# Performance work log

Hardware: AMD Instinct MI355X
Metric: run time of the kernel (lower is better)

Reference implementation:

```python
import jax, jax.numpy as jnp
import numpy as np
from jax import lax

START_IDX = 0
STOP_IDX = 1


def _forward_alg(feats_lbt, mask_lb, transitions):
    # feats_lbt: [L, B, T], mask_lb: [L, B], transitions[i, j] = score(j -> i)
    L, B, T = feats_lbt.shape
    init = jnp.full((B, T), -10000.0, dtype=feats_lbt.dtype).at[:, START_IDX].set(0.0)

    def step(fv, xs):
        feat, m = xs  # feat: [B, T], m: [B]
        # scores[b, next, prev] = fv[b, prev] + transitions[next, prev] + feat[b, next]
        scores = fv[:, None, :] + transitions[None, :, :] + feat[:, :, None]
        alphas = jax.nn.logsumexp(scores, axis=-1)  # [B, T]
        fv = jnp.where(m[:, None] > 0, alphas, fv)
        return fv, None

    fv, _ = lax.scan(step, init, (feats_lbt, mask_lb))
    terminal = fv + transitions[STOP_IDX][None, :]
    return jax.nn.logsumexp(terminal, axis=-1)  # [B]


def _score_sentence(feats_lbt, tags_bl, mask_lb, transitions):
    L, B, T = feats_lbt.shape
    start_col = jnp.full((B, 1), START_IDX, dtype=tags_bl.dtype)
    tags_ext = jnp.concatenate([start_col, tags_bl], axis=-1)  # [B, L+1]
    # transition scores along the gold path: [B, L]
    trans = transitions[tags_ext[:, 1:], tags_ext[:, :-1]]
    # emission scores: feats is [L, B, T] -> gather per-position gold tag
    emit = jnp.take_along_axis(
        feats_lbt, tags_bl.T[:, :, None], axis=-1
    )[:, :, 0]  # [L, B]
    step_scores = (trans.T + emit) * (mask_lb > 0)  # [L, B]
    score = step_scores.sum(axis=0)  # [B]
    lengths = mask_lb.sum(axis=0).astype(jnp.int32)  # [B]
    last_tag = tags_ext[jnp.arange(B), lengths]
    score = score + transitions[STOP_IDX, last_tag]
    return score


def setup_inputs() -> dict:
    key = jax.random.key(0)
    k1, k2, k3 = jax.random.split(key, 3)
    B, L, T = 256, 2048, 32
    efeats = jax.random.normal(k1, (B, L, T), dtype=jnp.float32)
    mask = jnp.ones((B, L), dtype=jnp.float32)
    tgt = jax.random.randint(k2, (B, L), 0, T, dtype=jnp.int32)
    transitions = jax.random.normal(k3, (T, T), dtype=jnp.float32)
    return {"efeats": efeats, "mask": mask, "tgt": tgt, "transitions": transitions}


def reference(efeats, mask, tgt, transitions):
    B, L = mask.shape
    mask_lb = mask.T  # [L, B]
    feats_lbt = jnp.transpose(efeats, (1, 0, 2))  # [L, B, T]
    forward_score = _forward_alg(feats_lbt, mask_lb, transitions)
    gold_score = _score_sentence(feats_lbt, tgt, mask_lb, transitions)
    loss = (forward_score - gold_score).sum() / B
    return loss
```

## Files before the change

kernel.cpp:

```cpp
#include <hip/hip_runtime.h>

#define B_SZ 256
#define L_SZ 2048
#define T_SZ 32
#define START_IDX 0
#define STOP_IDX 1

#define CLEN 64
#define NPAIR 32
#define NSLOT 8
#define NMAT_SEQ 4
#define NBLK_TOT (B_SZ * NMAT_SEQ)

#define FB_NCH 16
#define FB_CLEN 128

#define SCALE_LN 4.1588830833596718565f

typedef __attribute__((ext_vector_type(8))) short bf16x8;
typedef __attribute__((ext_vector_type(4))) float f32x4;
typedef __attribute__((ext_vector_type(2))) float f32x2;

__device__ __forceinline__ unsigned fau(float f){ union{float f; unsigned u;} v; v.f=f; return v.u; }
__device__ __forceinline__ float uaf(unsigned u){ union{unsigned u; float f;} v; v.u=u; return v.f; }
__device__ __forceinline__ int pack_trunc(float lo, float hi){
  return (int)__builtin_amdgcn_perm(fau(hi), fau(lo), 0x07060302u);
}
__device__ __forceinline__ bf16x8 frag_of(const int* p){
  union{ int i[4]; bf16x8 v; } u;
  u.i[0]=p[0]; u.i[1]=p[1]; u.i[2]=p[2]; u.i[3]=p[3];
  return u.v;
}

__device__ __forceinline__ void mfma4(bf16x8 A0, bf16x8 A1, bf16x8 B0, bf16x8 B1,
                                      f32x4& c00, f32x4& c01, f32x4& c10, f32x4& c11)
{
  const f32x4 z = {0.f,0.f,0.f,0.f};
  asm("s_nop 1\n\t"
      "v_mfma_f32_16x16x32_bf16 %0, %4, %5, %8\n\t"
      "v_mfma_f32_16x16x32_bf16 %1, %4, %6, %8\n\t"
      "v_mfma_f32_16x16x32_bf16 %2, %7, %5, %8\n\t"
      "v_mfma_f32_16x16x32_bf16 %3, %7, %6, %8\n\t"
      "s_nop 7\n\t"
      "s_nop 7"
      : "=&v"(c00), "=&v"(c01), "=&v"(c10), "=&v"(c11)
      : "v"(A0), "v"(B0), "v"(B1), "v"(A1), "v"(z));
}

__global__ void zero_kernel(float* out){ if(threadIdx.x==0) out[0]=0.f; }

__device__ __forceinline__ int mat_prod(const unsigned short* L, const unsigned short* Rt,
                                        unsigned short* dst, bool writeT, int lane)
{
  const int g = lane >> 4, c16 = lane & 15;
  const int ko = 8*g;
  bf16x8 A0 = *(const bf16x8*)(L  + (c16*T_SZ      + ko));
  bf16x8 A1 = *(const bf16x8*)(L  + ((16+c16)*T_SZ + ko));
  bf16x8 B0 = *(const bf16x8*)(Rt + (c16*T_SZ      + ko));
  bf16x8 B1 = *(const bf16x8*)(Rt + ((16+c16)*T_SZ + ko));
  f32x4 q00,q01,q10,q11;
  mfma4(A0, A1, B0, B1, q00, q01, q10, q11);

  unsigned mb = (unsigned)__builtin_amdgcn_readfirstlane((int)fau(q00[0]));
  int e = (int)((mb>>23)&255u) - 127;
  float r = uaf((unsigned)(127-e)<<23);
  #pragma unroll
  for (int i=0;i<4;++i){ q00[i]*=r; q01[i]*=r; q10[i]*=r; q11[i]*=r; }

  if (!writeT){
    #pragma unroll
    for (int reg=0; reg<4; ++reg){
      int x0 = 4*g + reg, x1 = 16 + 4*g + reg;
      dst[x0*T_SZ + c16]      = (unsigned short)(fau(q00[reg])>>16);
      dst[x0*T_SZ + 16 + c16] = (unsigned short)(fau(q01[reg])>>16);
      dst[x1*T_SZ + c16]      = (unsigned short)(fau(q10[reg])>>16);
      dst[x1*T_SZ + 16 + c16] = (unsigned short)(fau(q11[reg])>>16);
    }
  } else {
    #pragma unroll
    for (int rp=0; rp<2; ++rp){
      int xb0 = 4*g + 2*rp, xb1 = 16 + 4*g + 2*rp;
      *(int*)&dst[c16*T_SZ + xb0]        = pack_trunc(q00[2*rp], q00[2*rp+1]);
      *(int*)&dst[(16+c16)*T_SZ + xb0]   = pack_trunc(q01[2*rp], q01[2*rp+1]);
      *(int*)&dst[c16*T_SZ + xb1]        = pack_trunc(q10[2*rp], q10[2*rp+1]);
      *(int*)&dst[(16+c16)*T_SZ + xb1]   = pack_trunc(q11[2*rp], q11[2*rp+1]);
    }
  }
  return e;
}

__global__ __launch_bounds__(512, 8) void crf_chunk_kernel(
    const float* __restrict__ efeats, const float* __restrict__ mask,
    const int* __restrict__ tgt, const float* __restrict__ trans,
    unsigned short* __restrict__ wsM, int* __restrict__ wsE,
    float* __restrict__ wsG, float* __restrict__ wsL,
    float* __restrict__ out)
{
  __shared__ float s_trans[T_SZ*T_SZ];
  __shared__ float s_d[8][128];
  __shared__ unsigned short s_tree[NSLOT][T_SZ*T_SZ];
  __shared__ int   s_et[NSLOT];
  __shared__ float s_gd[8], s_ml[8];

  const int tid  = threadIdx.x;
  const int w    = tid >> 6;
  const int lane = tid & 63;
  const int g    = lane >> 4;
  const int c16  = lane & 15;

  const int b  = blockIdx.x >> 2;
  const int q  = blockIdx.x & 3;
  const int c  = q*NSLOT + w;
  const int l0 = c * CLEN;

  if (blockIdx.x == 0 && tid == 0) out[0] = 0.f;

  s_trans[tid]     = trans[tid];
  s_trans[tid+512] = trans[tid+512];
  __syncthreads();

  bf16x8 A0f, A1f;
  {
    int a0i[4], a1i[4];
    #pragma unroll
    for (int I=0; I<2; ++I){
      int row = 8*(c16>>2) + 4*I + (c16&3);
      float e[8];
      #pragma unroll
      for (int j=0;j<8;++j) e[j] = __expf(s_trans[row*T_SZ + 8*g + j]);
      int* dst = I ? a1i : a0i;
      #pragma unroll
      for (int p=0;p<4;++p) dst[p] = pack_trunc(e[2*p], e[2*p+1]);
    }
    A0f = frag_of(a0i); A1f = frag_of(a1i);
  }

  int b0[4], b1[4];
  #pragma unroll
  for (int p=0;p<4;++p){
    int s0 = 8*g + 2*p, s1 = s0+1;
    unsigned lo = (s0==c16)?0x3f80u:0u, hi = (s1==c16)?0x3f80u:0u;
    b0[p] = (int)(lo | (hi<<16));
    lo = (s0==16+c16)?0x3f80u:0u; hi = (s1==16+c16)?0x3f80u:0u;
    b1[p] = (int)(lo | (hi<<16));
  }

  const long fbase = ((long)b * L_SZ) * T_SZ;
  const int  mbase = b*L_SZ + l0;

  float mA = mask[mbase + lane];
  int   tA = tgt [mbase + lane];
  int   tpA = (l0 + lane == 0) ? START_IDX : tgt[mbase + lane - 1];

  float emA = efeats[fbase + (long)(l0+lane)*T_SZ + tA];
  float gl = (mA > 0.f) ? (s_trans[tA*T_SZ + tpA] + emA) : 0.f;
  float ml = mA;
  #pragma unroll
  for (int off=32; off>0; off>>=1){ gl += __shfl_xor(gl, off, 64); ml += __shfl_xor(ml, off, 64); }

  unsigned long long mb0 = __ballot(mA > 0.f);

  const float* fpt = efeats + fbase + (long)l0*T_SZ;
  float* s_dw = &s_d[w][0];

  float fq[4];
  #pragma unroll
  for (int i=1; i<=4; ++i) fq[i&3] = fpt[i*64 + lane];
  s_dw[lane] = __expf(fpt[lane] - SCALE_LN);

  if (mb0 == ~0ull){
    #pragma unroll 4
    for (int p=0; p<NPAIR; ++p){
      s_dw[((p+1)&1)*64 + lane] = __expf(fq[(p+1)&3] - SCALE_LN);
      int np = p+5; np = (np > NPAIR-1) ? (NPAIR-1) : np;
      fq[(p+1)&3] = fpt[np*64 + lane];
      const float* dbase = &s_dw[(p&1)*64];
      #pragma unroll
      for (int h=0; h<2; ++h){
        f32x4 c00,c01,c10,c11;
        mfma4(A0f, A1f, frag_of(b0), frag_of(b1), c00,c01,c10,c11);

        const float4* dv = (const float4*)(dbase + h*32);
        float4 dl = dv[2*g], dh2 = dv[2*g+1];
        f32x2 q0={c00[0],c00[1]}; q0 *= (f32x2){dl.x,dl.y};
        f32x2 q1={c00[2],c00[3]}; q1 *= (f32x2){dl.z,dl.w};
        f32x2 q2={c01[0],c01[1]}; q2 *= (f32x2){dl.x,dl.y};
        f32x2 q3={c01[2],c01[3]}; q3 *= (f32x2){dl.z,dl.w};
        f32x2 q4={c10[0],c10[1]}; q4 *= (f32x2){dh2.x,dh2.y};
        f32x2 q5={c10[2],c10[3]}; q5 *= (f32x2){dh2.z,dh2.w};
        f32x2 q6={c11[0],c11[1]}; q6 *= (f32x2){dh2.x,dh2.y};
        f32x2 q7={c11[2],c11[3]}; q7 *= (f32x2){dh2.z,dh2.w};

        b0[0]=pack_trunc(q0[0],q0[1]); b0[1]=pack_trunc(q1[0],q1[1]);
        b0[2]=pack_trunc(q4[0],q4[1]); b0[3]=pack_trunc(q5[0],q5[1]);
        b1[0]=pack_trunc(q2[0],q2[1]); b1[1]=pack_trunc(q3[0],q3[1]);
        b1[2]=pack_trunc(q6[0],q6[1]); b1[3]=pack_trunc(q7[0],q7[1]);
      }
    }
  } else {
    for (int p=0; p<NPAIR; ++p){
      s_dw[((p+1)&1)*64 + lane] = __expf(fq[(p+1)&3] - SCALE_LN);
      int np = p+5; if (np > NPAIR-1) np = NPAIR-1;
      fq[(p+1)&3] = fpt[np*64 + lane];
      const float* dbase = &s_dw[(p&1)*64];
      #pragma unroll
      for (int h=0; h<2; ++h){
        int t = 2*p + h;
        if ((mb0 >> t) & 1ull){
          f32x4 c00,c01,c10,c11;
          mfma4(A0f, A1f, frag_of(b0), frag_of(b1), c00,c01,c10,c11);

          const float4* dv = (const float4*)(dbase + h*32);
          float4 dl = dv[2*g], dh2 = dv[2*g+1];
          float f0=dl.x, f1=dl.y, f2=dl.z, f3=dl.w;
          float f4=dh2.x, f5=dh2.y, f6=dh2.z, f7=dh2.w;

          c00[0]*=f0; c00[1]*=f1; c00[2]*=f2; c00[3]*=f3;
          c01[0]*=f0; c01[1]*=f1; c01[2]*=f2; c01[3]*=f3;
          c10[0]*=f4; c10[1]*=f5; c10[2]*=f6; c10[3]*=f7;
          c11[0]*=f4; c11[1]*=f5; c11[2]*=f6; c11[3]*=f7;

          b0[0]=pack_trunc(c00[0],c00[1]); b0[1]=pack_trunc(c00[2],c00[3]);
          b0[2]=pack_trunc(c10[0],c10[1]); b0[3]=pack_trunc(c10[2],c10[3]);
          b1[0]=pack_trunc(c01[0],c01[1]); b1[1]=pack_trunc(c01[2],c01[3]);
          b1[2]=pack_trunc(c11[0],c11[1]); b1[3]=pack_trunc(c11[2],c11[3]);
        }
      }
    }
  }

  {
    unsigned short* S = &s_tree[w][0];
    if ((w & 1) == 0){
      #pragma unroll
      for (int p=0;p<4;++p){
        int s = 8*g + 2*p;
        *(int*)&S[c16*T_SZ + s]      = b0[p];
        *(int*)&S[(16+c16)*T_SZ + s] = b1[p];
      }
    } else {
      #pragma unroll
      for (int p=0;p<4;++p){
        int s = 8*g + 2*p;
        S[s*T_SZ + c16]          = (unsigned short)(b0[p] & 0xffff);
        S[(s+1)*T_SZ + c16]      = (unsigned short)(((unsigned)b0[p])>>16);
        S[s*T_SZ + 16 + c16]     = (unsigned short)(b1[p] & 0xffff);
        S[(s+1)*T_SZ + 16 + c16] = (unsigned short)(((unsigned)b1[p])>>16);
      }
    }
  }
  if (lane==0){
    s_et[w] = 6 * __popcll(mb0);
    s_gd[w] = gl; s_ml[w] = ml;
  }
  __syncthreads();

  if (w < 4){
    int e = mat_prod(&s_tree[2*w][0], &s_tree[2*w+1][0], &s_tree[2*w][0], (w&1)!=0, lane);
    if (lane==0) s_et[2*w] = s_et[2*w] + s_et[2*w+1] + e;
  }
  __syncthreads();
  if (w < 2){
    int e = mat_prod(&s_tree[4*w][0], &s_tree[4*w+2][0], &s_tree[4*w][0], (w&1)!=0, lane);
    if (lane==0) s_et[4*w] = s_et[4*w] + s_et[4*w+2] + e;
  }
  __syncthreads();
  if (w == 0){
    int e = mat_prod(&s_tree[0][0], &s_tree[4][0], &s_tree[0][0], false, lane);
    if (lane==0) s_et[0] = s_et[0] + s_et[4] + e;
  }
  __syncthreads();

  const int bid = blockIdx.x;
  ((int*)(wsM + (long)bid*(T_SZ*T_SZ)))[tid] = ((const int*)&s_tree[0][0])[tid];
  if (tid == 0){
    wsE[bid] = s_et[0];
    float gs=0.f, ls=0.f;
    #pragma unroll
    for (int i=0;i<8;++i){ gs += s_gd[i]; ls += s_ml[i]; }
    wsG[bid] = gs; wsL[bid] = ls;
  }
}

__global__ __launch_bounds__(64) void crf_combine_kernel(
    const unsigned short* __restrict__ wsM, const int* __restrict__ wsE,
    const float* __restrict__ wsG, const float* __restrict__ wsL,
    const int* __restrict__ tgt, const float* __restrict__ trans,
    float* __restrict__ out)
{
  __shared__ unsigned short sM[NMAT_SEQ*T_SZ*T_SZ];
  __shared__ float s_v[T_SZ];

  const int tid = threadIdx.x;
  const int b   = blockIdx.x;

  const uint4* src = (const uint4*)(wsM + (long)b*NMAT_SEQ*T_SZ*T_SZ);
  #pragma unroll
  for (int i=0;i<NMAT_SEQ*4;++i) ((uint4*)sM)[tid + i*64] = src[tid + i*64];
  __syncthreads();

  const int s = tid & 31;
  float v = (s==START_IDX)?1.f:0.f;
  int E = 0;
  #pragma unroll
  for (int j=0; j<NMAT_SEQ; ++j){
    if (tid < 32) s_v[s] = v;
    __syncthreads();
    const unsigned short* M = &sM[j*T_SZ*T_SZ];
    float u = 0.f;
    #pragma unroll 8
    for (int x=0; x<T_SZ; ++x){
      float mv = uaf(((unsigned)M[x*T_SZ + s])<<16);
      u = fmaf(mv, s_v[x], u);
    }
    unsigned ub = (unsigned)__builtin_amdgcn_readfirstlane((int)fau(u));
    int eu = (int)((ub>>23)&255u)-127;
    E += wsE[b*NMAT_SEQ + j] + eu;
    v = u * uaf((unsigned)(127-eu)<<23);
    __syncthreads();
  }
  float term = v * __expf(trans[STOP_IDX*T_SZ + s]);
  #pragma unroll
  for (int off=16; off>0; off>>=1) term += __shfl_xor(term, off, 32);
  float fwd = (float)E * 0.69314718055994530942f + __logf(term);

  if (tid == 0){
    float gp = 0.f, lp = 0.f;
    #pragma unroll
    for (int j=0;j<NMAT_SEQ;++j){ gp += wsG[b*NMAT_SEQ+j]; lp += wsL[b*NMAT_SEQ+j]; }
    int len = (int)lp;
    int last_tag = (len==0)? START_IDX : tgt[b*L_SZ + len-1];
    float goldT = gp + trans[STOP_IDX*T_SZ + last_tag];
    atomicAdd(out, (fwd - goldT) * (1.0f/B_SZ));
  }
}

__global__ __launch_bounds__(1024) void crf_loss_kernel(
    const float* __restrict__ efeats, const float* __restrict__ mask,
    const int* __restrict__ tgt, const float* __restrict__ trans,
    float* __restrict__ out)
{
  __shared__ float s_trans[T_SZ*T_SZ];
  __shared__ float s_d[FB_NCH][T_SZ];
  __shared__ unsigned short s_M[FB_NCH][T_SZ*T_SZ];
  __shared__ int   s_es[FB_NCH];
  __shared__ float s_gd[FB_NCH];
  __shared__ float s_mlv[FB_NCH];

  const int tid  = threadIdx.x;
  const int b    = blockIdx.x;
  const int w    = tid >> 6;
  const int lane = tid & 63;
  const int g    = lane >> 4;
  const int c16  = lane & 15;
  const int i32  = lane & 31;

  s_trans[tid] = trans[tid];
  __syncthreads();

  int a0[4], a1[4];
  #pragma unroll
  for (int I=0; I<2; ++I){
    int row = 8*(c16>>2) + 4*I + (c16&3);
    float e[8];
    #pragma unroll
    for (int j=0;j<8;++j) e[j] = __expf(s_trans[row*T_SZ + 8*g + j]);
    int* dst = I ? a1 : a0;
    #pragma unroll
    for (int p=0;p<4;++p) dst[p] = pack_trunc(e[2*p], e[2*p+1]);
  }

  int b0[4], b1[4];
  #pragma unroll
  for (int p=0;p<4;++p){
    int s0 = 8*g + 2*p, s1 = s0+1;
    unsigned lo = (s0==c16)?0x3f80u:0u, hi = (s1==c16)?0x3f80u:0u;
    b0[p] = (int)(lo | (hi<<16));
    lo = (s0==16+c16)?0x3f80u:0u; hi = (s1==16+c16)?0x3f80u:0u;
    b1[p] = (int)(lo | (hi<<16));
  }

  const int l0 = w * FB_CLEN;
  const long fbase = ((long)b * L_SZ) * T_SZ;

  float fqv[4];
  #pragma unroll
  for (int i=0;i<4;++i) fqv[i] = efeats[fbase + (long)(l0+i)*T_SZ + i32];

  int   tA = tgt [b*L_SZ + l0 + lane];
  int   tB = tgt [b*L_SZ + l0 + 64 + lane];
  float mA = mask[b*L_SZ + l0 + lane];
  float mB = mask[b*L_SZ + l0 + 64 + lane];
  int prev = (l0==0) ? START_IDX : tgt[b*L_SZ + l0 - 1];

  int esum = 0;
  float gold = 0.f, mlen = 0.f;
  const f32x4 zf = {0.f,0.f,0.f,0.f};

  #pragma unroll 4
  for (int t=0; t<FB_CLEN; ++t){
    float fcur = fqv[t&3];
    int lpf = l0 + t + 4; lpf = (lpf < L_SZ) ? lpf : (L_SZ-1);
    fqv[t&3] = efeats[fbase + (long)lpf*T_SZ + i32];

    float mk  = uaf((unsigned)__builtin_amdgcn_readlane((int)fau((t<64)?mA:mB), t&63));
    int   cur = __builtin_amdgcn_readlane((t<64)?tA:tB, t&63);
    mlen += mk;

    if (mk > 0.f){
      if (lane < 32) s_d[w][lane] = __expf(fcur);

      f32x4 c00 = __builtin_amdgcn_mfma_f32_16x16x32_bf16(frag_of(a0), frag_of(b0), zf, 0,0,0);
      f32x4 c01 = __builtin_amdgcn_mfma_f32_16x16x32_bf16(frag_of(a0), frag_of(b1), zf, 0,0,0);
      f32x4 c10 = __builtin_amdgcn_mfma_f32_16x16x32_bf16(frag_of(a1), frag_of(b0), zf, 0,0,0);
      f32x4 c11 = __builtin_amdgcn_mfma_f32_16x16x32_bf16(frag_of(a1), frag_of(b1), zf, 0,0,0);

      const float4* dv = (const float4*)(&s_d[w][0]);
      float4 dl = dv[2*g], dh = dv[2*g+1];
      float f0=dl.x, f1=dl.y, f2=dl.z, f3=dl.w;
      float f4=dh.x, f5=dh.y, f6=dh.z, f7=dh.w;

      float m00 = c00[0]*f0;
      unsigned mb = (unsigned)__builtin_amdgcn_readfirstlane((int)fau(m00));
      int e = (int)((mb>>23)&255u) - 127;
      esum += e;
      float r = uaf((unsigned)(127-e)<<23);
      f0*=r; f1*=r; f2*=r; f3*=r; f4*=r; f5*=r; f6*=r; f7*=r;

      c00[0]*=f0; c00[1]*=f1; c00[2]*=f2; c00[3]*=f3;
      c01[0]*=f0; c01[1]*=f1; c01[2]*=f2; c01[3]*=f3;
      c10[0]*=f4; c10[1]*=f5; c10[2]*=f6; c10[3]*=f7;
      c11[0]*=f4; c11[1]*=f5; c11[2]*=f6; c11[3]*=f7;

      b0[0]=pack_trunc(c00[0],c00[1]); b0[1]=pack_trunc(c00[2],c00[3]);
      b0[2]=pack_trunc(c10[0],c10[1]); b0[3]=pack_trunc(c10[2],c10[3]);
      b1[0]=pack_trunc(c01[0],c01[1]); b1[1]=pack_trunc(c01[2],c01[3]);
      b1[2]=pack_trunc(c11[0],c11[1]); b1[3]=pack_trunc(c11[2],c11[3]);

      float tp   = s_trans[cur*T_SZ + prev];
      float emit = uaf((unsigned)__builtin_amdgcn_readlane((int)fau(fcur), cur));
      gold += tp + emit;
    }
    prev = cur;
  }

  #pragma unroll
  for (int p=0;p<4;++p){
    int s = 8*g + 2*p;
    *(int*)((char*)(&s_M[w][0]) + (((long)(c16   )*T_SZ + s) * 2)) = b0[p];
    *(int*)((char*)(&s_M[w][0]) + (((long)(16+c16)*T_SZ + s) * 2)) = b1[p];
  }
  if (lane==0){ s_es[w]=esum; s_gd[w]=gold; s_mlv[w]=mlen; }
  __syncthreads();

  if (w==0){
    int s = i32;
    float v = (s==START_IDX)?1.f:0.f;
    int E = 0;
    for (int c=0;c<FB_NCH;++c){
      float u=0.f;
      #pragma unroll 8
      for (int k=0;k<T_SZ;++k){
        float mv = uaf(((unsigned)s_M[c][k*T_SZ + s])<<16);
        float vk = uaf((unsigned)__builtin_amdgcn_readlane((int)fau(v), k));
        u = fmaf(mv, vk, u);
      }
      unsigned ub = (unsigned)__builtin_amdgcn_readfirstlane((int)fau(u));
      int eu = (int)((ub>>23)&255u)-127;
      E += s_es[c] + eu;
      v = u * uaf((unsigned)(127-eu)<<23);
    }
    float term = v * __expf(s_trans[STOP_IDX*T_SZ + s]);
    #pragma unroll
    for (int off=16; off>0; off>>=1) term += __shfl_xor(term, off, 32);
    float fwd = (float)E * 0.69314718055994530942f + __logf(term);

    float gp = (s<FB_NCH)? s_gd[s] : 0.f;
    float lp = (s<FB_NCH)? s_mlv[s] : 0.f;
    #pragma unroll
    for (int off=16; off>0; off>>=1){ gp += __shfl_xor(gp, off, 32); lp += __shfl_xor(lp, off, 32); }
    int len = (int)lp;
    int last_tag = (len==0)? START_IDX : tgt[b*L_SZ + (len-1)];
    float goldT = gp + s_trans[STOP_IDX*T_SZ + last_tag];
    if (tid==0) atomicAdd(out, (fwd - goldT) * (1.0f/B_SZ));
  }
}

extern "C" void kernel_launch(void* const* d_in, const int* in_sizes, int n_in,
                              void* d_out, int out_size, void* d_ws, size_t ws_size,
                              hipStream_t stream)
{
  const float* efeats = (const float*)d_in[0];
  const float* mask   = (const float*)d_in[1];
  const int*   tgt    = (const int*)d_in[2];
  const float* trans  = (const float*)d_in[3];
  float* out = (float*)d_out;

  const size_t needM = (size_t)NBLK_TOT * T_SZ * T_SZ * 2;
  const size_t need  = needM + (size_t)NBLK_TOT * 12;

  if (ws_size >= need){
    unsigned short* wsM = (unsigned short*)d_ws;
    char* p = (char*)d_ws + needM;
    int*   wsE = (int*)p;
    float* wsG = (float*)(p + (size_t)NBLK_TOT*4);
    float* wsL = (float*)(p + (size_t)NBLK_TOT*8);
    crf_chunk_kernel<<<dim3(NBLK_TOT), dim3(512), 0, stream>>>(
        efeats, mask, tgt, trans, wsM, wsE, wsG, wsL, out);
    crf_combine_kernel<<<dim3(B_SZ), dim3(64), 0, stream>>>(
        wsM, wsE, wsG, wsL, tgt, trans, out);
  } else {
    zero_kernel<<<dim3(1), dim3(64), 0, stream>>>(out);
    crf_loss_kernel<<<dim3(B_SZ), dim3(1024), 0, stream>>>(efeats, mask, tgt, trans, out);
  }
}
```

Measured before the change: 139.4 us.

## Interleave two sequence chunks per wavefront to overlap MFMA dependency chains

Each wavefront now advances two independent 64-step chunks of the recurrence at once. A new 8-MFMA inline-asm block issues both chunks' matrix products back to back, so the fixed s_nop padding is shared between them. The chunk kernel now launches 256-thread blocks with half as many waves, and the first level of the tree reduction is done by every wave. The combine kernel's shared-memory copy loop is also halved so it matches the actual size of sM, which the old loop overran. The cost is more registers per wave and fewer waves for the scheduler to switch between.

```diff
diff --git a/kernel.cpp b/kernel.cpp
--- a/kernel.cpp
+++ b/kernel.cpp
@@ -47,6 +47,28 @@
       : "v"(A0), "v"(B0), "v"(B1), "v"(A1), "v"(z));
 }
 
+__device__ __forceinline__ void mfma8(bf16x8 A0, bf16x8 A1,
+                                      bf16x8 Ba0, bf16x8 Ba1, bf16x8 Bb0, bf16x8 Bb1,
+                                      f32x4& a00, f32x4& a01, f32x4& a10, f32x4& a11,
+                                      f32x4& b00, f32x4& b01, f32x4& b10, f32x4& b11)
+{
+  const f32x4 z = {0.f,0.f,0.f,0.f};
+  asm("s_nop 1\n\t"
+      "v_mfma_f32_16x16x32_bf16 %0, %8, %10, %14\n\t"
+      "v_mfma_f32_16x16x32_bf16 %1, %8, %11, %14\n\t"
+      "v_mfma_f32_16x16x32_bf16 %2, %9, %10, %14\n\t"
+      "v_mfma_f32_16x16x32_bf16 %3, %9, %11, %14\n\t"
+      "v_mfma_f32_16x16x32_bf16 %4, %8, %12, %14\n\t"
+      "v_mfma_f32_16x16x32_bf16 %5, %8, %13, %14\n\t"
+      "v_mfma_f32_16x16x32_bf16 %6, %9, %12, %14\n\t"
+      "v_mfma_f32_16x16x32_bf16 %7, %9, %13, %14\n\t"
+      "s_nop 7\n\t"
+      "s_nop 7"
+      : "=&v"(a00), "=&v"(a01), "=&v"(a10), "=&v"(a11),
+        "=&v"(b00), "=&v"(b01), "=&v"(b10), "=&v"(b11)
+      : "v"(A0), "v"(A1), "v"(Ba0), "v"(Ba1), "v"(Bb0), "v"(Bb1), "v"(z));
+}
+
 __global__ void zero_kernel(float* out){ if(threadIdx.x==0) out[0]=0.f; }
 
 __device__ __forceinline__ int mat_prod(const unsigned short* L, const unsigned short* Rt,
@@ -89,7 +111,7 @@
   return e;
 }
 
-__global__ __launch_bounds__(512, 8) void crf_chunk_kernel(
+__global__ __launch_bounds__(256, 4) void crf_chunk_kernel(
     const float* __restrict__ efeats, const float* __restrict__ mask,
     const int* __restrict__ tgt, const float* __restrict__ trans,
     unsigned short* __restrict__ wsM, int* __restrict__ wsE,
@@ -97,10 +119,10 @@
     float* __restrict__ out)
 {
   __shared__ float s_trans[T_SZ*T_SZ];
-  __shared__ float s_d[8][128];
+  __shared__ float s_d[4][256];
   __shared__ unsigned short s_tree[NSLOT][T_SZ*T_SZ];
   __shared__ int   s_et[NSLOT];
-  __shared__ float s_gd[8], s_ml[8];
+  __shared__ float s_gd[4], s_ml[4];
 
   const int tid  = threadIdx.x;
   const int w    = tid >> 6;
@@ -110,13 +132,13 @@
 
   const int b  = blockIdx.x >> 2;
   const int q  = blockIdx.x & 3;
-  const int c  = q*NSLOT + w;
-  const int l0 = c * CLEN;
+  const int l0A = q*(NSLOT*CLEN) + (2*w)*CLEN;
+  const int l0B = l0A + CLEN;
 
   if (blockIdx.x == 0 && tid == 0) out[0] = 0.f;
 
-  s_trans[tid]     = trans[tid];
-  s_trans[tid+512] = trans[tid+512];
+  #pragma unroll
+  for (int i=0;i<4;++i) s_trans[tid + i*256] = trans[tid + i*256];
   __syncthreads();
 
   bf16x8 A0f, A1f;
@@ -135,127 +157,174 @@
     A0f = frag_of(a0i); A1f = frag_of(a1i);
   }
 
-  int b0[4], b1[4];
+  int b0a[4], b1a[4], b0b[4], b1b[4];
   #pragma unroll
   for (int p=0;p<4;++p){
     int s0 = 8*g + 2*p, s1 = s0+1;
     unsigned lo = (s0==c16)?0x3f80u:0u, hi = (s1==c16)?0x3f80u:0u;
-    b0[p] = (int)(lo | (hi<<16));
+    b0a[p] = (int)(lo | (hi<<16));  b0b[p] = b0a[p];
     lo = (s0==16+c16)?0x3f80u:0u; hi = (s1==16+c16)?0x3f80u:0u;
-    b1[p] = (int)(lo | (hi<<16));
+    b1a[p] = (int)(lo | (hi<<16));  b1b[p] = b1a[p];
   }
 
   const long fbase = ((long)b * L_SZ) * T_SZ;
-  const int  mbase = b*L_SZ + l0;
-
-  float mA = mask[mbase + lane];
-  int   tA = tgt [mbase + lane];
-  int   tpA = (l0 + lane == 0) ? START_IDX : tgt[mbase + lane - 1];
-
-  float emA = efeats[fbase + (long)(l0+lane)*T_SZ + tA];
-  float gl = (mA > 0.f) ? (s_trans[tA*T_SZ + tpA] + emA) : 0.f;
-  float ml = mA;
+  const int  mbA = b*L_SZ + l0A;
+  const int  mbB = b*L_SZ + l0B;
+
+  float mA = mask[mbA + lane];
+  float mB = mask[mbB + lane];
+  int   tA = tgt [mbA + lane];
+  int   tB = tgt [mbB + lane];
+  int   tpA = (l0A + lane == 0) ? START_IDX : tgt[mbA + lane - 1];
+  int   tpB = tgt[mbB + lane - 1];
+
+  float emA = efeats[fbase + (long)(l0A+lane)*T_SZ + tA];
+  float emB = efeats[fbase + (long)(l0B+lane)*T_SZ + tB];
+  float gl = ((mA > 0.f) ? (s_trans[tA*T_SZ + tpA] + emA) : 0.f)
+           + ((mB > 0.f) ? (s_trans[tB*T_SZ + tpB] + emB) : 0.f);
+  float ml = mA + mB;
   #pragma unroll
   for (int off=32; off>0; off>>=1){ gl += __shfl_xor(gl, off, 64); ml += __shfl_xor(ml, off, 64); }
 
-  unsigned long long mb0 = __ballot(mA > 0.f);
-
-  const float* fpt = efeats + fbase + (long)l0*T_SZ;
-  float* s_dw = &s_d[w][0];
-
-  float fq[4];
-  #pragma unroll
-  for (int i=1; i<=4; ++i) fq[i&3] = fpt[i*64 + lane];
-  s_dw[lane] = __expf(fpt[lane] - SCALE_LN);
-
-  if (mb0 == ~0ull){
-    #pragma unroll 4
+  unsigned long long mba = __ballot(mA > 0.f);
+  unsigned long long mbb = __ballot(mB > 0.f);
+
+  const float* fptA = efeats + fbase + (long)l0A*T_SZ;
+  const float* fptB = efeats + fbase + (long)l0B*T_SZ;
+  float* s_dwA = &s_d[w][0];
+  float* s_dwB = &s_d[w][128];
+
+  float fqa[4], fqb[4];
+  #pragma unroll
+  for (int i=1; i<=4; ++i){ fqa[i&3] = fptA[i*64 + lane]; fqb[i&3] = fptB[i*64 + lane]; }
+  s_dwA[lane] = __expf(fptA[lane] - SCALE_LN);
+  s_dwB[lane] = __expf(fptB[lane] - SCALE_LN);
+
+  if ((mba & mbb) == ~0ull){
+    #pragma unroll 2
     for (int p=0; p<NPAIR; ++p){
-      s_dw[((p+1)&1)*64 + lane] = __expf(fq[(p+1)&3] - SCALE_LN);
+      s_dwA[((p+1)&1)*64 + lane] = __expf(fqa[(p+1)&3] - SCALE_LN);
+      s_dwB[((p+1)&1)*64 + lane] = __expf(fqb[(p+1)&3] - SCALE_LN);
       int np = p+5; np = (np > NPAIR-1) ? (NPAIR-1) : np;
-      fq[(p+1)&3] = fpt[np*64 + lane];
-      const float* dbase = &s_dw[(p&1)*64];
+      fqa[(p+1)&3] = fptA[np*64 + lane];
+      fqb[(p+1)&3] = fptB[np*64 + lane];
+      const float* dbA = &s_dwA[(p&1)*64];
+      const float* dbB = &s_dwB[(p&1)*64];
       #pragma unroll
       for (int h=0; h<2; ++h){
-        f32x4 c00,c01,c10,c11;
-        mfma4(A0f, A1f, frag_of(b0), frag_of(b1), c00,c01,c10,c11);
-
-        const float4* dv = (const float4*)(dbase + h*32);
-        float4 dl = dv[2*g], dh2 = dv[2*g+1];
-        f32x2 q0={c00[0],c00[1]}; q0 *= (f32x2){dl.x,dl.y};
-        f32x2 q1={c00[2],c00[3]}; q1 *= (f32x2){dl.z,dl.w};
-        f32x2 q2={c01[0],c01[1]}; q2 *= (f32x2){dl.x,dl.y};
-        f32x2 q3={c01[2],c01[3]}; q3 *= (f32x2){dl.z,dl.w};
-        f32x2 q4={c10[0],c10[1]}; q4 *= (f32x2){dh2.x,dh2.y};
-        f32x2 q5={c10[2],c10[3]}; q5 *= (f32x2){dh2.z,dh2.w};
-        f32x2 q6={c11[0],c11[1]}; q6 *= (f32x2){dh2.x,dh2.y};
-        f32x2 q7={c11[2],c11[3]}; q7 *= (f32x2){dh2.z,dh2.w};
-
-        b0[0]=pack_trunc(q0[0],q0[1]); b0[1]=pack_trunc(q1[0],q1[1]);
-        b0[2]=pack_trunc(q4[0],q4[1]); b0[3]=pack_trunc(q5[0],q5[1]);
-        b1[0]=pack_trunc(q2[0],q2[1]); b1[1]=pack_trunc(q3[0],q3[1]);
-        b1[2]=pack_trunc(q6[0],q6[1]); b1[3]=pack_trunc(q7[0],q7[1]);
+        f32x4 cA00,cA01,cA10,cA11, cB00,cB01,cB10,cB11;
+        mfma8(A0f, A1f, frag_of(b0a), frag_of(b1a), frag_of(b0b), frag_of(b1b),
+              cA00,cA01,cA10,cA11, cB00,cB01,cB10,cB11);
+
+        const float4* dvA = (const float4*)(dbA + h*32);
+        const float4* dvB = (const float4*)(dbB + h*32);
+        float4 dlA = dvA[2*g], dhA = dvA[2*g+1];
+        float4 dlB = dvB[2*g], dhB = dvB[2*g+1];
+
+        {
+          f32x2 q0={cA00[0],cA00[1]}; q0 *= (f32x2){dlA.x,dlA.y};
+          f32x2 q1={cA00[2],cA00[3]}; q1 *= (f32x2){dlA.z,dlA.w};
+          f32x2 q2={cA01[0],cA01[1]}; q2 *= (f32x2){dlA.x,dlA.y};
+          f32x2 q3={cA01[2],cA01[3]}; q3 *= (f32x2){dlA.z,dlA.w};
+          f32x2 q4={cA10[0],cA10[1]}; q4 *= (f32x2){dhA.x,dhA.y};
+          f32x2 q5={cA10[2],cA10[3]}; q5 *= (f32x2){dhA.z,dhA.w};
+          f32x2 q6={cA11[0],cA11[1]}; q6 *= (f32x2){dhA.x,dhA.y};
+          f32x2 q7={cA11[2],cA11[3]}; q7 *= (f32x2){dhA.z,dhA.w};
+          b0a[0]=pack_trunc(q0[0],q0[1]); b0a[1]=pack_trunc(q1[0],q1[1]);
+          b0a[2]=pack_trunc(q4[0],q4[1]); b0a[3]=pack_trunc(q5[0],q5[1]);
+          b1a[0]=pack_trunc(q2[0],q2[1]); b1a[1]=pack_trunc(q3[0],q3[1]);
+          b1a[2]=pack_trunc(q6[0],q6[1]); b1a[3]=pack_trunc(q7[0],q7[1]);
+        }
+        {
+          f32x2 q0={cB00[0],cB00[1]}; q0 *= (f32x2){dlB.x,dlB.y};
+          f32x2 q1={cB00[2],cB00[3]}; q1 *= (f32x2){dlB.z,dlB.w};
+          f32x2 q2={cB01[0],cB01[1]}; q2 *= (f32x2){dlB.x,dlB.y};
+          f32x2 q3={cB01[2],cB01[3]}; q3 *= (f32x2){dlB.z,dlB.w};
+          f32x2 q4={cB10[0],cB10[1]}; q4 *= (f32x2){dhB.x,dhB.y};
+          f32x2 q5={cB10[2],cB10[3]}; q5 *= (f32x2){dhB.z,dhB.w};
+          f32x2 q6={cB11[0],cB11[1]}; q6 *= (f32x2){dhB.x,dhB.y};
+          f32x2 q7={cB11[2],cB11[3]}; q7 *= (f32x2){dhB.z,dhB.w};
+          b0b[0]=pack_trunc(q0[0],q0[1]); b0b[1]=pack_trunc(q1[0],q1[1]);
+          b0b[2]=pack_trunc(q4[0],q4[1]); b0b[3]=pack_trunc(q5[0],q5[1]);
+          b1b[0]=pack_trunc(q2[0],q2[1]); b1b[1]=pack_trunc(q3[0],q3[1]);
+          b1b[2]=pack_trunc(q6[0],q6[1]); b1b[3]=pack_trunc(q7[0],q7[1]);
+        }
       }
     }
   } else {
     for (int p=0; p<NPAIR; ++p){
-      s_dw[((p+1)&1)*64 + lane] = __expf(fq[(p+1)&3] - SCALE_LN);
+      s_dwA[((p+1)&1)*64 + lane] = __expf(fqa[(p+1)&3] - SCALE_LN);
+      s_dwB[((p+1)&1)*64 + lane] = __expf(fqb[(p+1)&3] - SCALE_LN);
       int np = p+5; if (np > NPAIR-1) np = NPAIR-1;
-      fq[(p+1)&3] = fpt[np*64 + lane];
-      const float* dbase = &s_dw[(p&1)*64];
+      fqa[(p+1)&3] = fptA[np*64 + lane];
+      fqb[(p+1)&3] = fptB[np*64 + lane];
+      const float* dbA = &s_dwA[(p&1)*64];
+      const float* dbB = &s_dwB[(p&1)*64];
       #pragma unroll
       for (int h=0; h<2; ++h){
         int t = 2*p + h;
-        if ((mb0 >> t) & 1ull){
-          f32x4 c00,c01,c10,c11;
-          mfma4(A0f, A1f, frag_of(b0), frag_of(b1), c00,c01,c10,c11);
-
-          const float4* dv = (const float4*)(dbase + h*32);
-          float4 dl = dv[2*g], dh2 = dv[2*g+1];
+        f32x4 cA00,cA01,cA10,cA11, cB00,cB01,cB10,cB11;
+        mfma8(A0f, A1f, frag_of(b0a), frag_of(b1a), frag_of(b0b), frag_of(b1b),
+              cA00,cA01,cA10,cA11, cB00,cB01,cB10,cB11);
+
+        if ((mba >> t) & 1ull){
+          const float4* dvA = (const float4*)(dbA + h*32);
+          float4 dl = dvA[2*g], dh2 = dvA[2*g+1];
           float f0=dl.x, f1=dl.y, f2=dl.z, f3=dl.w;
           float f4=dh2.x, f5=dh2.y, f6=dh2.z, f7=dh2.w;
-
-          c00[0]*=f0; c00[1]*=f1; c00[2]*=f2; c00[3]*=f3;
-          c01[0]*=f0; c01[1]*=f1; c01[2]*=f2; c01[3]*=f3;
-          c10[0]*=f4; c10[1]*=f5; c10[2]*=f6; c10[3]*=f7;
-          c11[0]*=f4; c11[1]*=f5; c11[2]*=f6; c11[3]*=f7;
-
-          b0[0]=pack_trunc(c00[0],c00[1]); b0[1]=pack_trunc(c00[2],c00[3]);
-          b0[2]=pack_trunc(c10[0],c10[1]); b0[3]=pack_trunc(c10[2],c10[3]);
-          b1[0]=pack_trunc(c01[0],c01[1]); b1[1]=pack_trunc(c01[2],c01[3]);
-          b1[2]=pack_trunc(c11[0],c11[1]); b1[3]=pack_trunc(c11[2],c11[3]);
+          cA00[0]*=f0; cA00[1]*=f1; cA00[2]*=f2; cA00[3]*=f3;
+          cA01[0]*=f0; cA01[1]*=f1; cA01[2]*=f2; cA01[3]*=f3;
+          cA10[0]*=f4; cA10[1]*=f5; cA10[2]*=f6; cA10[3]*=f7;
+          cA11[0]*=f4; cA11[1]*=f5; cA11[2]*=f6; cA11[3]*=f7;
+          b0a[0]=pack_trunc(cA00[0],cA00[1]); b0a[1]=pack_trunc(cA00[2],cA00[3]);
+          b0a[2]=pack_trunc(cA10[0],cA10[1]); b0a[3]=pack_trunc(cA10[2],cA10[3]);
+          b1a[0]=pack_trunc(cA01[0],cA01[1]); b1a[1]=pack_trunc(cA01[2],cA01[3]);
+          b1a[2]=pack_trunc(cA11[0],cA11[1]); b1a[3]=pack_trunc(cA11[2],cA11[3]);
+        }
+        if ((mbb >> t) & 1ull){
+          const float4* dvB = (const float4*)(dbB + h*32);
+          float4 dl = dvB[2*g], dh2 = dvB[2*g+1];
+          float f0=dl.x, f1=dl.y, f2=dl.z, f3=dl.w;
+          float f4=dh2.x, f5=dh2.y, f6=dh2.z, f7=dh2.w;
+          cB00[0]*=f0; cB00[1]*=f1; cB00[2]*=f2; cB00[3]*=f3;
+          cB01[0]*=f0; cB01[1]*=f1; cB01[2]*=f2; cB01[3]*=f3;
+          cB10[0]*=f4; cB10[1]*=f5; cB10[2]*=f6; cB10[3]*=f7;
+          cB11[0]*=f4; cB11[1]*=f5; cB11[2]*=f6; cB11[3]*=f7;
+          b0b[0]=pack_trunc(cB00[0],cB00[1]); b0b[1]=pack_trunc(cB00[2],cB00[3]);
+          b0b[2]=pack_trunc(cB10[0],cB10[1]); b0b[3]=pack_trunc(cB10[2],cB10[3]);
+          b1b[0]=pack_trunc(cB01[0],cB01[1]); b1b[1]=pack_trunc(cB01[2],cB01[3]);
+          b1b[2]=pack_trunc(cB11[0],cB11[1]); b1b[3]=pack_trunc(cB11[2],cB11[3]);
         }
       }
     }
   }
 
   {
-    unsigned short* S = &s_tree[w][0];
-    if ((w & 1) == 0){
-      #pragma unroll
-      for (int p=0;p<4;++p){
-        int s = 8*g + 2*p;
-        *(int*)&S[c16*T_SZ + s]      = b0[p];
-        *(int*)&S[(16+c16)*T_SZ + s] = b1[p];
-      }
-    } else {
-      #pragma unroll
-      for (int p=0;p<4;++p){
-        int s = 8*g + 2*p;
-        S[s*T_SZ + c16]          = (unsigned short)(b0[p] & 0xffff);
-        S[(s+1)*T_SZ + c16]      = (unsigned short)(((unsigned)b0[p])>>16);
-        S[s*T_SZ + 16 + c16]     = (unsigned short)(b1[p] & 0xffff);
-        S[(s+1)*T_SZ + 16 + c16] = (unsigned short)(((unsigned)b1[p])>>16);
-      }
+    unsigned short* S = &s_tree[2*w][0];
+    #pragma unroll
+    for (int p=0;p<4;++p){
+      int s = 8*g + 2*p;
+      *(int*)&S[c16*T_SZ + s]      = b0a[p];
+      *(int*)&S[(16+c16)*T_SZ + s] = b1a[p];
+    }
+    unsigned short* St = &s_tree[2*w+1][0];
+    #pragma unroll
+    for (int p=0;p<4;++p){
+      int s = 8*g + 2*p;
+      St[s*T_SZ + c16]          = (unsigned short)(b0b[p] & 0xffff);
+      St[(s+1)*T_SZ + c16]      = (unsigned short)(((unsigned)b0b[p])>>16);
+      St[s*T_SZ + 16 + c16]     = (unsigned short)(b1b[p] & 0xffff);
+      St[(s+1)*T_SZ + 16 + c16] = (unsigned short)(((unsigned)b1b[p])>>16);
     }
   }
   if (lane==0){
-    s_et[w] = 6 * __popcll(mb0);
+    s_et[2*w]   = 6 * __popcll(mba);
+    s_et[2*w+1] = 6 * __popcll(mbb);
     s_gd[w] = gl; s_ml[w] = ml;
   }
   __syncthreads();
 
-  if (w < 4){
+  {
     int e = mat_prod(&s_tree[2*w][0], &s_tree[2*w+1][0], &s_tree[2*w][0], (w&1)!=0, lane);
     if (lane==0) s_et[2*w] = s_et[2*w] + s_et[2*w+1] + e;
   }
@@ -272,12 +341,13 @@
   __syncthreads();
 
   const int bid = blockIdx.x;
-  ((int*)(wsM + (long)bid*(T_SZ*T_SZ)))[tid] = ((const int*)&s_tree[0][0])[tid];
+  ((int*)(wsM + (long)bid*(T_SZ*T_SZ)))[tid]       = ((const int*)&s_tree[0][0])[tid];
+  ((int*)(wsM + (long)bid*(T_SZ*T_SZ)))[tid + 256] = ((const int*)&s_tree[0][0])[tid + 256];
   if (tid == 0){
     wsE[bid] = s_et[0];
     float gs=0.f, ls=0.f;
     #pragma unroll
-    for (int i=0;i<8;++i){ gs += s_gd[i]; ls += s_ml[i]; }
+    for (int i=0;i<4;++i){ gs += s_gd[i]; ls += s_ml[i]; }
     wsG[bid] = gs; wsL[bid] = ls;
   }
 }
@@ -296,7 +366,7 @@
 
   const uint4* src = (const uint4*)(wsM + (long)b*NMAT_SEQ*T_SZ*T_SZ);
   #pragma unroll
-  for (int i=0;i<NMAT_SEQ*4;++i) ((uint4*)sM)[tid + i*64] = src[tid + i*64];
+  for (int i=0;i<NMAT_SEQ*2;++i) ((uint4*)sM)[tid + i*64] = src[tid + i*64];
   __syncthreads();
 
   const int s = tid & 31;
@@ -505,7 +575,7 @@
     int*   wsE = (int*)p;
     float* wsG = (float*)(p + (size_t)NBLK_TOT*4);
     float* wsL = (float*)(p + (size_t)NBLK_TOT*8);
-    crf_chunk_kernel<<<dim3(NBLK_TOT), dim3(512), 0, stream>>>(
+    crf_chunk_kernel<<<dim3(NBLK_TOT), dim3(256), 0, stream>>>(
         efeats, mask, tgt, trans, wsM, wsE, wsG, wsL, out);
     crf_combine_kernel<<<dim3(B_SZ), dim3(64), 0, stream>>>(
         wsM, wsE, wsG, wsL, tgt, trans, out);
```

Result: no change. 141.1 us (+1.2%).

## Fold emission scaling into per-step MFMA A operand on the full-mask path

Applied to the files above, without the earlier changes.

On the all-unmasked fast path, each step now builds the A operand as diag(exp(emission)) times exp(transitions). The emission rows are loaded directly into registers, so the shared-memory staging of exp(emission), its reads and the post-MFMA multiplies drop out of the serial step chain. Each iteration handles one timestep instead of a pair. A operands for the next step are computed ahead, overlapping with the current MFMA. The change also relaxes launch bounds from 8 to 4 waves, and shrinks the combine kernel's copy loop to match the shared buffer size, which fixes a previous overrun.

```diff
diff --git a/kernel.cpp b/kernel.cpp
--- a/kernel.cpp
+++ b/kernel.cpp
@@ -19,7 +19,6 @@
 
 typedef __attribute__((ext_vector_type(8))) short bf16x8;
 typedef __attribute__((ext_vector_type(4))) float f32x4;
-typedef __attribute__((ext_vector_type(2))) float f32x2;
 
 __device__ __forceinline__ unsigned fau(float f){ union{float f; unsigned u;} v; v.f=f; return v.u; }
 __device__ __forceinline__ float uaf(unsigned u){ union{unsigned u; float f;} v; v.u=u; return v.f; }
@@ -89,7 +88,7 @@
   return e;
 }
 
-__global__ __launch_bounds__(512, 8) void crf_chunk_kernel(
+__global__ __launch_bounds__(512, 4) void crf_chunk_kernel(
     const float* __restrict__ efeats, const float* __restrict__ mask,
     const int* __restrict__ tgt, const float* __restrict__ trans,
     unsigned short* __restrict__ wsM, int* __restrict__ wsE,
@@ -119,20 +118,12 @@
   s_trans[tid+512] = trans[tid+512];
   __syncthreads();
 
-  bf16x8 A0f, A1f;
-  {
-    int a0i[4], a1i[4];
-    #pragma unroll
-    for (int I=0; I<2; ++I){
-      int row = 8*(c16>>2) + 4*I + (c16&3);
-      float e[8];
-      #pragma unroll
-      for (int j=0;j<8;++j) e[j] = __expf(s_trans[row*T_SZ + 8*g + j]);
-      int* dst = I ? a1i : a0i;
-      #pragma unroll
-      for (int p=0;p<4;++p) dst[p] = pack_trunc(e[2*p], e[2*p+1]);
-    }
-    A0f = frag_of(a0i); A1f = frag_of(a1i);
+  const int row0 = 8*(c16>>2) + (c16&3);
+  float e0[8], e1[8];
+  #pragma unroll
+  for (int j=0;j<8;++j){
+    e0[j] = __expf(s_trans[row0*T_SZ     + 8*g + j]);
+    e1[j] = __expf(s_trans[(row0+4)*T_SZ + 8*g + j]);
   }
 
   int b0[4], b1[4];
@@ -161,43 +152,64 @@
   unsigned long long mb0 = __ballot(mA > 0.f);
 
   const float* fpt = efeats + fbase + (long)l0*T_SZ;
-  float* s_dw = &s_d[w][0];
-
-  float fq[4];
-  #pragma unroll
-  for (int i=1; i<=4; ++i) fq[i&3] = fpt[i*64 + lane];
-  s_dw[lane] = __expf(fpt[lane] - SCALE_LN);
 
   if (mb0 == ~0ull){
+    float fr0[4], fr4[4];
+    #pragma unroll
+    for (int i=0;i<4;++i){
+      fr0[i] = fpt[i*T_SZ + row0];
+      fr4[i] = fpt[i*T_SZ + row0 + 4];
+    }
+    int a0s[4], a1s[4];
+    {
+      float d0 = __expf(fr0[0] - SCALE_LN), d1 = __expf(fr4[0] - SCALE_LN);
+      #pragma unroll
+      for (int p=0;p<4;++p){
+        a0s[p] = pack_trunc(e0[2*p]*d0, e0[2*p+1]*d0);
+        a1s[p] = pack_trunc(e1[2*p]*d1, e1[2*p+1]*d1);
+      }
+    }
+
     #pragma unroll 4
-    for (int p=0; p<NPAIR; ++p){
-      s_dw[((p+1)&1)*64 + lane] = __expf(fq[(p+1)&3] - SCALE_LN);
-      int np = p+5; np = (np > NPAIR-1) ? (NPAIR-1) : np;
-      fq[(p+1)&3] = fpt[np*64 + lane];
-      const float* dbase = &s_dw[(p&1)*64];
+    for (int t=0; t<CLEN; ++t){
+      int a0n[4], a1n[4];
+      {
+        float d0 = __expf(fr0[(t+1)&3] - SCALE_LN), d1 = __expf(fr4[(t+1)&3] - SCALE_LN);
+        #pragma unroll
+        for (int p=0;p<4;++p){
+          a0n[p] = pack_trunc(e0[2*p]*d0, e0[2*p+1]*d0);
+          a1n[p] = pack_trunc(e1[2*p]*d1, e1[2*p+1]*d1);
+        }
+      }
+      int tp4 = t+4; tp4 = (tp4 > CLEN-1) ? (CLEN-1) : tp4;
+      fr0[t&3] = fpt[tp4*T_SZ + row0];
+      fr4[t&3] = fpt[tp4*T_SZ + row0 + 4];
+
+      f32x4 c00,c01,c10,c11;
+      mfma4(frag_of(a0s), frag_of(a1s), frag_of(b0), frag_of(b1), c00,c01,c10,c11);
+      b0[0]=pack_trunc(c00[0],c00[1]); b0[1]=pack_trunc(c00[2],c00[3]);
+      b0[2]=pack_trunc(c10[0],c10[1]); b0[3]=pack_trunc(c10[2],c10[3]);
+      b1[0]=pack_trunc(c01[0],c01[1]); b1[1]=pack_trunc(c01[2],c01[3]);
+      b1[2]=pack_trunc(c11[0],c11[1]); b1[3]=pack_trunc(c11[2],c11[3]);
+
       #pragma unroll
-      for (int h=0; h<2; ++h){
-        f32x4 c00,c01,c10,c11;
-        mfma4(A0f, A1f, frag_of(b0), frag_of(b1), c00,c01,c10,c11);
-
-        const float4* dv = (const float4*)(dbase + h*32);
-        float4 dl = dv[2*g], dh2 = dv[2*g+1];
-        f32x2 q0={c00[0],c00[1]}; q0 *= (f32x2){dl.x,dl.y};
-        f32x2 q1={c00[2],c00[3]}; q1 *= (f32x2){dl.z,dl.w};
-        f32x2 q2={c01[0],c01[1]}; q2 *= (f32x2){dl.x,dl.y};
-        f32x2 q3={c01[2],c01[3]}; q3 *= (f32x2){dl.z,dl.w};
-        f32x2 q4={c10[0],c10[1]}; q4 *= (f32x2){dh2.x,dh2.y};
-        f32x2 q5={c10[2],c10[3]}; q5 *= (f32x2){dh2.z,dh2.w};
-        f32x2 q6={c11[0],c11[1]}; q6 *= (f32x2){dh2.x,dh2.y};
-        f32x2 q7={c11[2],c11[3]}; q7 *= (f32x2){dh2.z,dh2.w};
-
-        b0[0]=pack_trunc(q0[0],q0[1]); b0[1]=pack_trunc(q1[0],q1[1]);
-        b0[2]=pack_trunc(q4[0],q4[1]); b0[3]=pack_trunc(q5[0],q5[1]);
-        b1[0]=pack_trunc(q2[0],q2[1]); b1[1]=pack_trunc(q3[0],q3[1]);
-        b1[2]=pack_trunc(q6[0],q6[1]); b1[3]=pack_trunc(q7[0],q7[1]);
-      }
+      for (int p=0;p<4;++p){ a0s[p]=a0n[p]; a1s[p]=a1n[p]; }
     }
   } else {
+    int a0c[4], a1c[4];
+    #pragma unroll
+    for (int p=0;p<4;++p){
+      a0c[p] = pack_trunc(e0[2*p], e0[2*p+1]);
+      a1c[p] = pack_trunc(e1[2*p], e1[2*p+1]);
+    }
+    bf16x8 A0f = frag_of(a0c), A1f = frag_of(a1c);
+
+    float* s_dw = &s_d[w][0];
+    float fq[4];
+    #pragma unroll
+    for (int i=1; i<=4; ++i) fq[i&3] = fpt[i*64 + lane];
+    s_dw[lane] = __expf(fpt[lane] - SCALE_LN);
+
     for (int p=0; p<NPAIR; ++p){
       s_dw[((p+1)&1)*64 + lane] = __expf(fq[(p+1)&3] - SCALE_LN);
       int np = p+5; if (np > NPAIR-1) np = NPAIR-1;
@@ -296,7 +308,7 @@
 
   const uint4* src = (const uint4*)(wsM + (long)b*NMAT_SEQ*T_SZ*T_SZ);
   #pragma unroll
-  for (int i=0;i<NMAT_SEQ*4;++i) ((uint4*)sM)[tid + i*64] = src[tid + i*64];
+  for (int i=0;i<NMAT_SEQ*2;++i) ((uint4*)sM)[tid + i*64] = src[tid + i*64];
   __syncthreads();
 
   const int s = tid & 31;
```

New measurement: 142.0 us. Within noise of the previous version (+1.9%).

## Fuse combine step into chunk kernel via last-block atomic counter

Applied to the files above, without the earlier changes.

Removes the separate combine kernel launch. Each chunk block now bumps a global counter after a threadfence, and the last block to finish combines all 256 sequences, using readlane broadcasts instead of shared memory. The fast-path scaling also drops the packed f32x2 multiplies for scalar multiplies. This saves a launch and its gap, but puts all 256 combines on one block of 8 waves, which could serialize the tail, and it adds a memset launch.

```diff
diff --git a/kernel.cpp b/kernel.cpp
--- a/kernel.cpp
+++ b/kernel.cpp
@@ -19,7 +19,6 @@
 
 typedef __attribute__((ext_vector_type(8))) short bf16x8;
 typedef __attribute__((ext_vector_type(4))) float f32x4;
-typedef __attribute__((ext_vector_type(2))) float f32x2;
 
 __device__ __forceinline__ unsigned fau(float f){ union{float f; unsigned u;} v; v.f=f; return v.u; }
 __device__ __forceinline__ float uaf(unsigned u){ union{unsigned u; float f;} v; v.u=u; return v.f; }
@@ -94,6 +93,7 @@
     const int* __restrict__ tgt, const float* __restrict__ trans,
     unsigned short* __restrict__ wsM, int* __restrict__ wsE,
     float* __restrict__ wsG, float* __restrict__ wsL,
+    int* __restrict__ wsC,
     float* __restrict__ out)
 {
   __shared__ float s_trans[T_SZ*T_SZ];
@@ -101,6 +101,7 @@
   __shared__ unsigned short s_tree[NSLOT][T_SZ*T_SZ];
   __shared__ int   s_et[NSLOT];
   __shared__ float s_gd[8], s_ml[8];
+  __shared__ int   s_last;
 
   const int tid  = threadIdx.x;
   const int w    = tid >> 6;
@@ -112,8 +113,6 @@
   const int q  = blockIdx.x & 3;
   const int c  = q*NSLOT + w;
   const int l0 = c * CLEN;
-
-  if (blockIdx.x == 0 && tid == 0) out[0] = 0.f;
 
   s_trans[tid]     = trans[tid];
   s_trans[tid+512] = trans[tid+512];
@@ -182,19 +181,18 @@
 
         const float4* dv = (const float4*)(dbase + h*32);
         float4 dl = dv[2*g], dh2 = dv[2*g+1];
-        f32x2 q0={c00[0],c00[1]}; q0 *= (f32x2){dl.x,dl.y};
-        f32x2 q1={c00[2],c00[3]}; q1 *= (f32x2){dl.z,dl.w};
-        f32x2 q2={c01[0],c01[1]}; q2 *= (f32x2){dl.x,dl.y};
-        f32x2 q3={c01[2],c01[3]}; q3 *= (f32x2){dl.z,dl.w};
-        f32x2 q4={c10[0],c10[1]}; q4 *= (f32x2){dh2.x,dh2.y};
-        f32x2 q5={c10[2],c10[3]}; q5 *= (f32x2){dh2.z,dh2.w};
-        f32x2 q6={c11[0],c11[1]}; q6 *= (f32x2){dh2.x,dh2.y};
-        f32x2 q7={c11[2],c11[3]}; q7 *= (f32x2){dh2.z,dh2.w};
-
-        b0[0]=pack_trunc(q0[0],q0[1]); b0[1]=pack_trunc(q1[0],q1[1]);
-        b0[2]=pack_trunc(q4[0],q4[1]); b0[3]=pack_trunc(q5[0],q5[1]);
-        b1[0]=pack_trunc(q2[0],q2[1]); b1[1]=pack_trunc(q3[0],q3[1]);
-        b1[2]=pack_trunc(q6[0],q6[1]); b1[3]=pack_trunc(q7[0],q7[1]);
+        float f0=dl.x, f1=dl.y, f2=dl.z, f3=dl.w;
+        float f4=dh2.x, f5=dh2.y, f6=dh2.z, f7=dh2.w;
+
+        c00[0]*=f0; c00[1]*=f1; c00[2]*=f2; c00[3]*=f3;
+        c01[0]*=f0; c01[1]*=f1; c01[2]*=f2; c01[3]*=f3;
+        c10[0]*=f4; c10[1]*=f5; c10[2]*=f6; c10[3]*=f7;
+        c11[0]*=f4; c11[1]*=f5; c11[2]*=f6; c11[3]*=f7;
+
+        b0[0]=pack_trunc(c00[0],c00[1]); b0[1]=pack_trunc(c00[2],c00[3]);
+        b0[2]=pack_trunc(c10[0],c10[1]); b0[3]=pack_trunc(c10[2],c10[3]);
+        b1[0]=pack_trunc(c01[0],c01[1]); b1[1]=pack_trunc(c01[2],c01[3]);
+        b1[2]=pack_trunc(c11[0],c11[1]); b1[3]=pack_trunc(c11[2],c11[3]);
       }
     }
   } else {
@@ -280,58 +278,53 @@
     for (int i=0;i<8;++i){ gs += s_gd[i]; ls += s_ml[i]; }
     wsG[bid] = gs; wsL[bid] = ls;
   }
-}
-
-__global__ __launch_bounds__(64) void crf_combine_kernel(
-    const unsigned short* __restrict__ wsM, const int* __restrict__ wsE,
-    const float* __restrict__ wsG, const float* __restrict__ wsL,
-    const int* __restrict__ tgt, const float* __restrict__ trans,
-    float* __restrict__ out)
-{
-  __shared__ unsigned short sM[NMAT_SEQ*T_SZ*T_SZ];
-  __shared__ float s_v[T_SZ];
-
-  const int tid = threadIdx.x;
-  const int b   = blockIdx.x;
-
-  const uint4* src = (const uint4*)(wsM + (long)b*NMAT_SEQ*T_SZ*T_SZ);
-  #pragma unroll
-  for (int i=0;i<NMAT_SEQ*4;++i) ((uint4*)sM)[tid + i*64] = src[tid + i*64];
-  __syncthreads();
-
-  const int s = tid & 31;
-  float v = (s==START_IDX)?1.f:0.f;
-  int E = 0;
-  #pragma unroll
-  for (int j=0; j<NMAT_SEQ; ++j){
-    if (tid < 32) s_v[s] = v;
-    __syncthreads();
-    const unsigned short* M = &sM[j*T_SZ*T_SZ];
-    float u = 0.f;
-    #pragma unroll 8
-    for (int x=0; x<T_SZ; ++x){
-      float mv = uaf(((unsigned)M[x*T_SZ + s])<<16);
-      u = fmaf(mv, s_v[x], u);
-    }
-    unsigned ub = (unsigned)__builtin_amdgcn_readfirstlane((int)fau(u));
-    int eu = (int)((ub>>23)&255u)-127;
-    E += wsE[b*NMAT_SEQ + j] + eu;
-    v = u * uaf((unsigned)(127-eu)<<23);
-    __syncthreads();
-  }
-  float term = v * __expf(trans[STOP_IDX*T_SZ + s]);
-  #pragma unroll
-  for (int off=16; off>0; off>>=1) term += __shfl_xor(term, off, 32);
-  float fwd = (float)E * 0.69314718055994530942f + __logf(term);
-
+
+  __threadfence();
   if (tid == 0){
-    float gp = 0.f, lp = 0.f;
-    #pragma unroll
-    for (int j=0;j<NMAT_SEQ;++j){ gp += wsG[b*NMAT_SEQ+j]; lp += wsL[b*NMAT_SEQ+j]; }
-    int len = (int)lp;
-    int last_tag = (len==0)? START_IDX : tgt[b*L_SZ + len-1];
-    float goldT = gp + trans[STOP_IDX*T_SZ + last_tag];
-    atomicAdd(out, (fwd - goldT) * (1.0f/B_SZ));
+    int done = atomicAdd(wsC, 1);
+    s_last = (done == NBLK_TOT - 1) ? 1 : 0;
+  }
+  __syncthreads();
+  if (s_last == 0) return;
+  __threadfence();
+
+  if (tid == 0) out[0] = 0.f;
+  __syncthreads();
+
+  const int s32 = lane & 31;
+  for (int sq = w; sq < B_SZ; sq += 8){
+    const unsigned short* Mb = wsM + (long)sq * NMAT_SEQ * (T_SZ*T_SZ);
+    float v = (s32==START_IDX) ? 1.f : 0.f;
+    int E = 0;
+    #pragma unroll
+    for (int j=0; j<NMAT_SEQ; ++j){
+      const unsigned short* M = Mb + j*(T_SZ*T_SZ);
+      float u = 0.f;
+      #pragma unroll 8
+      for (int x=0; x<T_SZ; ++x){
+        float mv = uaf(((unsigned)M[x*T_SZ + s32])<<16);
+        float vx = uaf((unsigned)__builtin_amdgcn_readlane((int)fau(v), x));
+        u = fmaf(mv, vx, u);
+      }
+      unsigned ub = (unsigned)__builtin_amdgcn_readfirstlane((int)fau(u));
+      int eu = (int)((ub>>23)&255u)-127;
+      E += wsE[sq*NMAT_SEQ + j] + eu;
+      v = u * uaf((unsigned)(127-eu)<<23);
+    }
+    float term = v * __expf(s_trans[STOP_IDX*T_SZ + s32]);
+    #pragma unroll
+    for (int off=16; off>0; off>>=1) term += __shfl_xor(term, off, 32);
+    float fwd = (float)E * 0.69314718055994530942f + __logf(term);
+
+    if (lane == 0){
+      float gp = 0.f, lp = 0.f;
+      #pragma unroll
+      for (int j=0;j<NMAT_SEQ;++j){ gp += wsG[sq*NMAT_SEQ+j]; lp += wsL[sq*NMAT_SEQ+j]; }
+      int len = (int)lp;
+      int last_tag = (len==0)? START_IDX : tgt[sq*L_SZ + len-1];
+      float goldT = gp + s_trans[STOP_IDX*T_SZ + last_tag];
+      atomicAdd(out, (fwd - goldT) * (1.0f/B_SZ));
+    }
   }
 }
 
@@ -497,7 +490,8 @@
   float* out = (float*)d_out;
 
   const size_t needM = (size_t)NBLK_TOT * T_SZ * T_SZ * 2;
-  const size_t need  = needM + (size_t)NBLK_TOT * 12;
+  const size_t scOff = needM + (size_t)NBLK_TOT * 12;
+  const size_t need  = scOff + 4;
 
   if (ws_size >= need){
     unsigned short* wsM = (unsigned short*)d_ws;
@@ -505,10 +499,10 @@
     int*   wsE = (int*)p;
     float* wsG = (float*)(p + (size_t)NBLK_TOT*4);
     float* wsL = (float*)(p + (size_t)NBLK_TOT*8);
+    int*   wsC = (int*)((char*)d_ws + scOff);
+    hipMemsetAsync(wsC, 0, 4, stream);
     crf_chunk_kernel<<<dim3(NBLK_TOT), dim3(512), 0, stream>>>(
-        efeats, mask, tgt, trans, wsM, wsE, wsG, wsL, out);
-    crf_combine_kernel<<<dim3(B_SZ), dim3(64), 0, stream>>>(
-        wsM, wsE, wsG, wsL, tgt, trans, out);
+        efeats, mask, tgt, trans, wsM, wsE, wsG, wsL, wsC, out);
   } else {
     zero_kernel<<<dim3(1), dim3(64), 0, stream>>>(out);
     crf_loss_kernel<<<dim3(B_SZ), dim3(1024), 0, stream>>>(efeats, mask, tgt, trans, out);
```

New measurement: 482.6 us. 3.46x slower.
